# Kernel optimization log

Measured on AMD Instinct MI355X. Metric: run time of the kernel, lower is better.

Reference implementation:

```python
import jax, jax.numpy as jnp
import numpy as np

N_EMBD = 256
B, T = 2, 512


def setup_inputs() -> dict:
    key = jax.random.key(0)
    kx, ks, kv = jax.random.split(key, 3)
    x = jax.random.normal(kx, (B, T, N_EMBD), dtype=jnp.float32)
    # init std 0.02 per nn.init.normal_(..., std=0.02); keeps I - scaled well-conditioned
    skew_param = 0.02 * jax.random.normal(ks, (N_EMBD, N_EMBD), dtype=jnp.float32)
    vector = 0.02 * jax.random.normal(kv, (1, N_EMBD), dtype=jnp.float32)
    return {"x": x, "skew_param": skew_param, "vector": vector}


def reference(x, skew_param, vector):
    n = skew_param.shape[0]
    skew = skew_param - skew_param.T                      # (n, n), skew-symmetric
    # scaled[b,t,i,j] = x[b,t,i] * skew[i,j]  -> (B, T, n, n)
    scaled = x[..., :, None] * skew
    eye = jnp.eye(n, dtype=x.dtype)
    # Cayley transform: (I - scaled)^{-1} (I + scaled), batched over (B, T)
    q = jnp.linalg.solve(eye - scaled, eye + scaled)      # (B, T, n, n)
    # (1, n) @ (B, T, n, n) -> (B, T, n) after squeezing the row dim
    out = jnp.einsum('n,btnm->btm', vector[0], q)
    return out
```

## Files before the change

### kernel.cpp

```cpp
#include <hip/hip_runtime.h>
#include <math.h>

#define N 256
#define G 4
#define BLK 1024
#define S1 12
#define S2 10
#define SP1 13
#define VS 268
#define UTS 280
#define RIDGE 3e-5f

typedef _Float16 half8v __attribute__((ext_vector_type(8)));
typedef float float4v __attribute__((ext_vector_type(4)));

#define OFF_K     0
#define OFF_UT0   55744
#define OFF_UT1   57984
#define OFF_ZTW   60224
#define OFF_GRAM  64320
#define OFF_INVN  67024
#define OFF_L     67232
#define OFF_D     69536
#define ARENA_SZ  69728

#define LD_FRAG(base, t) (*(const half8v*)((base) + (mn & 3) * UTS + 32 * (t) + 8 * mq))

#define MATVEC(basep, dst) do {                                                        \
    float4v acc0 = {0.f, 0.f, 0.f, 0.f};                                               \
    float4v acc1 = {0.f, 0.f, 0.f, 0.f};                                               \
    _Pragma("unroll")                                                                  \
    for (int t = 0; t < 4; ++t) {                                                      \
        acc0 = __builtin_amdgcn_mfma_f32_16x16x32_f16(Shi[t], LD_FRAG(basep, t), acc0, 0, 0, 0);          \
        acc1 = __builtin_amdgcn_mfma_f32_16x16x32_f16(Shi[t + 4], LD_FRAG(basep, t + 4), acc1, 0, 0, 0);  \
    }                                                                                  \
    float4v accs = acc0 + acc1;                                                        \
    if (mn < 4) *(float4v*)(zTw + wv * 64 + mn * 16 + mq * 4) = accs;                  \
    dst = zTw[wv * 64 + g * 16 + coff];                                                \
} while (0)

__global__ __launch_bounds__(BLK, 4) void cayley_v11(const float* __restrict__ x_all,
                                                     const float* __restrict__ P,
                                                     const float* __restrict__ v_in,
                                                     float* __restrict__ out, int batch) {
    __shared__ __align__(16) char arena[ARENA_SZ];
    float* sK      = (float*)(arena + OFF_K);
    _Float16* uT0  = (_Float16*)(arena + OFF_UT0);
    _Float16* uT1  = (_Float16*)(arena + OFF_UT1);
    float* zTw     = (float*)(arena + OFF_ZTW);
    float* sGram   = (float*)(arena + OFF_GRAM);
    float* sInvN   = (float*)(arena + OFF_INVN);
    float* sL      = (float*)(arena + OFF_L);
    float* sD      = (float*)(arena + OFF_D);

    const int tid = threadIdx.x;
    const int lane = tid & 63, wv = tid >> 6;
    const int mn = lane & 15, mq = lane >> 4;
    const int c = tid >> 2, g = tid & 3;
    const int coff = lane >> 2;
    const int sys = blockIdx.x * G + g;
    const bool alive = sys < batch;

    half8v Shi[8];
    {
        const int r = 16 * wv + mn;
#pragma unroll
        for (int t = 0; t < 8; ++t) {
            const int k0 = 32 * t + 8 * mq;
            float4v pa = *(const float4v*)(P + r * N + k0);
            float4v pb = *(const float4v*)(P + r * N + k0 + 4);
            half8v hi;
            hi[0] = (_Float16)(pa.x - P[(k0 + 0) * N + r]);
            hi[1] = (_Float16)(pa.y - P[(k0 + 1) * N + r]);
            hi[2] = (_Float16)(pa.z - P[(k0 + 2) * N + r]);
            hi[3] = (_Float16)(pa.w - P[(k0 + 3) * N + r]);
            hi[4] = (_Float16)(pb.x - P[(k0 + 4) * N + r]);
            hi[5] = (_Float16)(pb.y - P[(k0 + 5) * N + r]);
            hi[6] = (_Float16)(pb.z - P[(k0 + 6) * N + r]);
            hi[7] = (_Float16)(pb.w - P[(k0 + 7) * N + r]);
            Shi[t] = hi;
        }
    }

    const float x_own = alive ? x_all[sys * N + c] : 0.f;
    const float v_own = v_in[c];
    float wsol = 0.f;

    for (int sw = 0; sw < 2; ++sw) {
        const int s = sw ? S2 : S1;

        float kq;
        if (sw == 0) {
            kq = alive ? v_own : 0.f;
        } else {
            uT1[g * UTS + c] = (_Float16)(x_own * wsol);
            __syncthreads();
            float zm;
            MATVEC(uT1, zm);
            kq = alive ? (v_own - wsol - zm) : 0.f;
        }
        sK[g * VS + c] = kq;
        uT0[g * UTS + c] = (_Float16)(x_own * kq);
        __syncthreads();

        for (int i = 1; i <= s; ++i) {
            float zm;
            if (i & 1) { MATVEC(uT0, zm); } else { MATVEC(uT1, zm); }
            kq += zm;
            sK[(i * G + g) * VS + c] = kq;
            if (i < s) {
                _Float16* dst = (i & 1) ? uT1 : uT0;
                dst[g * UTS + c] = (_Float16)(x_own * kq);
            }
            __syncthreads();
        }

        const int NP = (s + 1) * (s + 2) / 2;
        for (int pp = wv; pp < NP; pp += 16) {
            int i = 0, rem = pp;
            while (rem >= (s + 1 - i)) { rem -= (s + 1 - i); ++i; }
            const int j = i + rem;
            const int gq = lane >> 4, q = lane & 15;
            const float* ka = sK + (i * G + gq) * VS + 16 * q;
            const float* kb = sK + (j * G + gq) * VS + 16 * q;
            float p;
            {
                float4v a0 = *(const float4v*)(ka);
                float4v b0 = *(const float4v*)(kb);
                float4v a1 = *(const float4v*)(ka + 4);
                float4v b1 = *(const float4v*)(kb + 4);
                p = a0.x * b0.x;
                p = fmaf(a0.y, b0.y, p); p = fmaf(a0.z, b0.z, p); p = fmaf(a0.w, b0.w, p);
                p = fmaf(a1.x, b1.x, p); p = fmaf(a1.y, b1.y, p);
                p = fmaf(a1.z, b1.z, p); p = fmaf(a1.w, b1.w, p);
            }
            {
                float4v a0 = *(const float4v*)(ka + 8);
                float4v b0 = *(const float4v*)(kb + 8);
                float4v a1 = *(const float4v*)(ka + 12);
                float4v b1 = *(const float4v*)(kb + 12);
                p = fmaf(a0.x, b0.x, p); p = fmaf(a0.y, b0.y, p);
                p = fmaf(a0.z, b0.z, p); p = fmaf(a0.w, b0.w, p);
                p = fmaf(a1.x, b1.x, p); p = fmaf(a1.y, b1.y, p);
                p = fmaf(a1.z, b1.z, p); p = fmaf(a1.w, b1.w, p);
            }
            p += __shfl_xor(p, 1); p += __shfl_xor(p, 2);
            p += __shfl_xor(p, 4); p += __shfl_xor(p, 8);
            if (q == 0) {
                sGram[(i * SP1 + j) * G + gq] = p;
                if (i != j) sGram[(j * SP1 + i) * G + gq] = p;
            }
        }
        __syncthreads();

        if (tid < 4 * (s + 1)) {
            const int i = tid >> 2, gq = tid & 3;
            const float dii = sGram[(i * SP1 + i) * G + gq];
            sInvN[i * G + gq] = (dii > 1e-30f) ? (1.f / sqrtf(dii)) : 0.f;
        }
        __syncthreads();

        if (wv < 4) {
            const int gq = wv;
            const int rr = lane;
            const float inv_r = (rr < s) ? sInvN[(rr + 1) * G + gq] : 0.f;
            for (int k = 0; k < s; ++k) {
                float a = 0.f;
                if (rr >= k && rr < s) {
                    a = (rr == k) ? (1.f + RIDGE)
                                  : sGram[((rr + 1) * SP1 + (k + 1)) * G + gq]
                                        * inv_r * sInvN[(k + 1) * G + gq];
                    for (int m = 0; m < k; ++m)
                        a = fmaf(-sL[(rr * S1 + m) * G + gq],
                                 sL[(k * S1 + m) * G + gq], a);
                }
                float dk = __shfl(a, k);
                dk = fmaxf(dk, 0.5f * RIDGE);
                const float invd = 1.f / sqrtf(dk);
                if (rr >= k && rr < s) sL[(rr * S1 + k) * G + gq] = a * invd;
            }
            float trr = 0.f, acc = 0.f;
            const float rhs = (rr < s)
                ? sGram[((rr + 1) * SP1) * G + gq] * inv_r * sInvN[gq] : 0.f;
            for (int k = 0; k < s; ++k) {
                const float Lkk = sL[(k * S1 + k) * G + gq];
                float tk = (Lkk > 1e-20f) ? (rhs - acc) / Lkk : 0.f;
                tk = __shfl(tk, k);
                if (rr == k) trr = tk;
                if (rr > k && rr < s)
                    acc = fmaf(sL[(rr * S1 + k) * G + gq], tk, acc);
            }
            float crr = 0.f;
            acc = 0.f;
            for (int k = s - 1; k >= 0; --k) {
                const float Lkk = sL[(k * S1 + k) * G + gq];
                float ck = (Lkk > 1e-20f) ? (trr - acc) / Lkk : 0.f;
                ck = __shfl(ck, k);
                if (rr == k) crr = ck;
                if (rr < k) acc = fmaf(sL[(k * S1 + rr) * G + gq], ck, acc);
            }
            if (rr < s) {
                const float n0 = sqrtf(fmaxf(sGram[0 * G + gq], 0.f));
                sD[rr * G + gq] = n0 * crr * sInvN[(rr + 1) * G + gq];
            }
        }
        __syncthreads();

        for (int i = 0; i < s; ++i)
            wsol = fmaf(sD[i * G + g], sK[(i * G + g) * VS + c], wsol);
        __syncthreads();
    }

    if (alive) out[sys * N + c] = 2.f * wsol - v_own;
}

extern "C" void kernel_launch(void* const* d_in, const int* in_sizes, int n_in,
                              void* d_out, int out_size, void* d_ws, size_t ws_size,
                              hipStream_t stream) {
    const float* x = (const float*)d_in[0];
    const float* P = (const float*)d_in[1];
    const float* v = (const float*)d_in[2];
    float* out = (float*)d_out;
    const int batch = in_sizes[0] / N;

    const int nblk = (batch + G - 1) / G;
    hipLaunchKernelGGL(cayley_v11, dim3(nblk), dim3(BLK), 0, stream, x, P, v, out, batch);
}
```

Measured before the change: 103.5 us.

## Switch Krylov basis to scaled powers and shrink subspace dimension

The iterative solver's Krylov vectors are now pure scaled powers (k_i = 0.5·M k_{i-1}) instead of accumulated sums. The normal equations are rebuilt from the Gram matrix of these vectors using linear combinations that stand for the old (I+M)-style basis. Separate norm computation and one barrier are removed. The subspace sizes S1/S2 are reduced, which cuts matvecs and Gram work per sweep and shrinks shared memory, at the risk of lower accuracy from fewer basis vectors.

Measured after the change: 97.76 us. -5.5%, faster.

```diff
diff --git a/kernel.cpp b/kernel.cpp
--- a/kernel.cpp
+++ b/kernel.cpp
@@ -4,9 +4,9 @@
 #define N 256
 #define G 4
 #define BLK 1024
-#define S1 12
-#define S2 10
-#define SP1 13
+#define S1 10
+#define S2 8
+#define SP1 11
 #define VS 268
 #define UTS 280
 #define RIDGE 3e-5f
@@ -15,14 +15,13 @@
 typedef float float4v __attribute__((ext_vector_type(4)));
 
 #define OFF_K     0
-#define OFF_UT0   55744
-#define OFF_UT1   57984
-#define OFF_ZTW   60224
-#define OFF_GRAM  64320
-#define OFF_INVN  67024
-#define OFF_L     67232
-#define OFF_D     69536
-#define ARENA_SZ  69728
+#define OFF_UT0   47168
+#define OFF_UT1   49408
+#define OFF_ZTW   51648
+#define OFF_GRAM  55744
+#define OFF_L     57680
+#define OFF_D     59280
+#define ARENA_SZ  59456
 
 #define LD_FRAG(base, t) (*(const half8v*)((base) + (mn & 3) * UTS + 32 * (t) + 8 * mq))
 
@@ -39,7 +38,7 @@
     dst = zTw[wv * 64 + g * 16 + coff];                                                \
 } while (0)
 
-__global__ __launch_bounds__(BLK, 4) void cayley_v11(const float* __restrict__ x_all,
+__global__ __launch_bounds__(BLK, 4) void cayley_v12(const float* __restrict__ x_all,
                                                      const float* __restrict__ P,
                                                      const float* __restrict__ v_in,
                                                      float* __restrict__ out, int batch) {
@@ -49,7 +48,6 @@
     _Float16* uT1  = (_Float16*)(arena + OFF_UT1);
     float* zTw     = (float*)(arena + OFF_ZTW);
     float* sGram   = (float*)(arena + OFF_GRAM);
-    float* sInvN   = (float*)(arena + OFF_INVN);
     float* sL      = (float*)(arena + OFF_L);
     float* sD      = (float*)(arena + OFF_D);
 
@@ -106,7 +104,7 @@
         for (int i = 1; i <= s; ++i) {
             float zm;
             if (i & 1) { MATVEC(uT0, zm); } else { MATVEC(uT1, zm); }
-            kq += zm;
+            kq = 0.5f * zm;
             sK[(i * G + g) * VS + c] = kq;
             if (i < s) {
                 _Float16* dst = (i & 1) ? uT1 : uT0;
@@ -153,23 +151,27 @@
         }
         __syncthreads();
 
-        if (tid < 4 * (s + 1)) {
-            const int i = tid >> 2, gq = tid & 3;
-            const float dii = sGram[(i * SP1 + i) * G + gq];
-            sInvN[i * G + gq] = (dii > 1e-30f) ? (1.f / sqrtf(dii)) : 0.f;
-        }
-        __syncthreads();
-
         if (wv < 4) {
             const int gq = wv;
             const int rr = lane;
-            const float inv_r = (rr < s) ? sInvN[(rr + 1) * G + gq] : 0.f;
+#define GG(i, j) sGram[((i) * SP1 + (j)) * G + gq]
+            float invn_r = 0.f;
+            if (rr < s) {
+                const float Brr = GG(rr, rr) + 4.f * GG(rr, rr + 1)
+                                + 4.f * GG(rr + 1, rr + 1);
+                invn_r = (Brr > 1e-30f) ? (1.f / sqrtf(Brr)) : 0.f;
+            }
             for (int k = 0; k < s; ++k) {
+                const float invn_k = __shfl(invn_r, k);
                 float a = 0.f;
                 if (rr >= k && rr < s) {
-                    a = (rr == k) ? (1.f + RIDGE)
-                                  : sGram[((rr + 1) * SP1 + (k + 1)) * G + gq]
-                                        * inv_r * sInvN[(k + 1) * G + gq];
+                    if (rr == k) {
+                        a = 1.f + RIDGE;
+                    } else {
+                        const float Brk = GG(rr, k) + 2.f * GG(rr, k + 1)
+                                        + 2.f * GG(rr + 1, k) + 4.f * GG(rr + 1, k + 1);
+                        a = Brk * invn_r * invn_k;
+                    }
                     for (int m = 0; m < k; ++m)
                         a = fmaf(-sL[(rr * S1 + m) * G + gq],
                                  sL[(k * S1 + m) * G + gq], a);
@@ -181,7 +183,8 @@
             }
             float trr = 0.f, acc = 0.f;
             const float rhs = (rr < s)
-                ? sGram[((rr + 1) * SP1) * G + gq] * inv_r * sInvN[gq] : 0.f;
+                ? (GG(rr, 0) + 2.f * GG(rr + 1, 0)) * invn_r : 0.f;
+#undef GG
             for (int k = 0; k < s; ++k) {
                 const float Lkk = sL[(k * S1 + k) * G + gq];
                 float tk = (Lkk > 1e-20f) ? (rhs - acc) / Lkk : 0.f;
@@ -199,10 +202,7 @@
                 if (rr == k) crr = ck;
                 if (rr < k) acc = fmaf(sL[(k * S1 + rr) * G + gq], ck, acc);
             }
-            if (rr < s) {
-                const float n0 = sqrtf(fmaxf(sGram[0 * G + gq], 0.f));
-                sD[rr * G + gq] = n0 * crr * sInvN[(rr + 1) * G + gq];
-            }
+            if (rr < s) sD[rr * G + gq] = crr * invn_r;
         }
         __syncthreads();
 
@@ -224,5 +224,5 @@
     const int batch = in_sizes[0] / N;
 
     const int nblk = (batch + G - 1) / G;
-    hipLaunchKernelGGL(cayley_v11, dim3(nblk), dim3(BLK), 0, stream, x, P, v, out, batch);
+    hipLaunchKernelGGL(cayley_v12, dim3(nblk), dim3(BLK), 0, stream, x, P, v, out, batch);
 }
```
